# Performance work log

Measured on AMD Instinct MI355X. Metric: run time of the kernel, lower is better.

## Reference

```python
import jax, jax.numpy as jnp
import numpy as np

N_BINS = 25


def setup_inputs() -> dict:
    key = jax.random.key(0)
    k1, k2 = jax.random.split(key)
    logits = jax.random.normal(k1, (500000, 100), dtype=jnp.float32)
    labels = jax.random.randint(k2, (500000,), 0, 100, dtype=jnp.int64)
    return {"logits": logits, "labels": labels}


def reference(logits, labels):
    # softmax confidences + predictions
    probs = jax.nn.softmax(logits, axis=1)
    confidences = jnp.max(probs, axis=1)              # [N]
    predictions = jnp.argmax(probs, axis=1)           # [N]
    accuracies = (predictions == labels).astype(jnp.float32)

    # Equal-width bins over (0,1]: bin i covers (i/n_bins, (i+1)/n_bins].
    # conf > lower AND conf <= upper  <=>  bin = ceil(conf*n_bins)-1 (conf>0 always for softmax).
    bins = jnp.clip(jnp.ceil(confidences * N_BINS).astype(jnp.int32) - 1, 0, N_BINS - 1)

    counts = jax.ops.segment_sum(jnp.ones_like(confidences), bins, num_segments=N_BINS)
    sum_conf = jax.ops.segment_sum(confidences, bins, num_segments=N_BINS)
    sum_acc = jax.ops.segment_sum(accuracies, bins, num_segments=N_BINS)

    n = jnp.float32(confidences.shape[0])
    prop_in_bin = counts / n
    safe_counts = jnp.maximum(counts, 1.0)
    avg_conf = sum_conf / safe_counts
    avg_acc = sum_acc / safe_counts

    ece = jnp.sum(jnp.where(counts > 0, jnp.abs(avg_conf - avg_acc) * prop_in_bin, 0.0))
    return ece
```

## Files before the change

kernel.cpp:

```cpp
#include <hip/hip_runtime.h>
#include <cfloat>

#define NBINS 25
#define RPB   128
#define THREADS 256
#define GRID1 1024

__launch_bounds__(THREADS, 3)
__global__ void ece_pass1(const float* __restrict__ logits,
                          const int* __restrict__ labels,
                          float* __restrict__ part, int n) {
    __shared__ float tile[RPB * 100];
    __shared__ float s_cnt[NBINS], s_conf[NBINS], s_acc[NBINS];
    const int t = threadIdx.x;
    if (t < NBINS) { s_cnt[t] = 0.f; s_conf[t] = 0.f; s_acc[t] = 0.f; }

    const int j = t & 3;
    const int g = t >> 2;

    for (int c = blockIdx.x; c * RPB < n; c += GRID1) {
        const int base = c * RPB;
        const int rows = min(RPB, n - base);
        const int nf4  = rows * 25;

        const float4* src = reinterpret_cast<const float4*>(logits) + (size_t)base * 25;
        float4* dst = reinterpret_cast<float4*>(tile);
#pragma unroll
        for (int k = 0; k < 13; ++k) {
            const int idx = t + k * THREADS;
            if (idx < nf4) dst[idx] = src[idx];
        }
        __syncthreads();

#pragma unroll
        for (int rr = 0; rr < RPB; rr += 64) {
            const int r = rr + g;
            const float* rowp = tile + r * 100;
            float4 v[6];
#pragma unroll
            for (int k = 0; k < 6; ++k)
                v[k] = *reinterpret_cast<const float4*>(rowp + (j + 4 * k) * 4);
            const float x24 = rowp[96 + j];

            float m = v[0].x; int mi = 4 * j;
            if (v[0].y > m) { m = v[0].y; mi = 4 * j + 1; }
            if (v[0].z > m) { m = v[0].z; mi = 4 * j + 2; }
            if (v[0].w > m) { m = v[0].w; mi = 4 * j + 3; }
#pragma unroll
            for (int k = 1; k < 6; ++k) {
                const int idx = 4 * (j + 4 * k);
                if (v[k].x > m) { m = v[k].x; mi = idx; }
                if (v[k].y > m) { m = v[k].y; mi = idx + 1; }
                if (v[k].z > m) { m = v[k].z; mi = idx + 2; }
                if (v[k].w > m) { m = v[k].w; mi = idx + 3; }
            }
            if (x24 > m) { m = x24; mi = 96 + j; }
#pragma unroll
            for (int off = 1; off <= 2; off <<= 1) {
                const float om = __shfl_xor(m, off);
                const int   oi = __shfl_xor(mi, off);
                if (om > m || (om == m && oi < mi)) { m = om; mi = oi; }
            }
            float s = __expf(x24 - m);
#pragma unroll
            for (int k = 0; k < 6; ++k) {
                s += __expf(v[k].x - m) + __expf(v[k].y - m) +
                     __expf(v[k].z - m) + __expf(v[k].w - m);
            }
#pragma unroll
            for (int off = 1; off <= 2; off <<= 1) s += __shfl_xor(s, off);

            if (j == 0 && r < rows) {
                const float conf = 1.0f / s;
                int bin = (int)ceilf(conf * (float)NBINS) - 1;
                bin = min(max(bin, 0), NBINS - 1);
                const float acc = (mi == labels[base + r]) ? 1.f : 0.f;
                atomicAdd(&s_cnt[bin], 1.f);
                atomicAdd(&s_conf[bin], conf);
                atomicAdd(&s_acc[bin], acc);
            }
        }
        __syncthreads();
    }

    if (t < NBINS) {
        part[t * GRID1 + blockIdx.x]               = s_cnt[t];
        part[(NBINS + t) * GRID1 + blockIdx.x]     = s_conf[t];
        part[(2 * NBINS + t) * GRID1 + blockIdx.x] = s_acc[t];
    }
}

__global__ void ece_final(const float* __restrict__ part, float* __restrict__ out, float n) {
    __shared__ float sacc[3 * NBINS];
    const int t = threadIdx.x;
    const int wave = t >> 6, lane = t & 63;
    for (int slot = wave; slot < 3 * NBINS; slot += 16) {
        const float* p = part + slot * GRID1;
        float s = 0.f;
        for (int k = lane; k < GRID1; k += 64) s += p[k];
#pragma unroll
        for (int off = 32; off; off >>= 1) s += __shfl_xor(s, off);
        if (lane == 0) sacc[slot] = s;
    }
    __syncthreads();
    if (t < 64) {
        float term = 0.f;
        if (t < NBINS) {
            const float cnt = sacc[t];
            const float sc  = sacc[NBINS + t];
            const float sa  = sacc[2 * NBINS + t];
            if (cnt > 0.f) {
                const float inv = 1.f / cnt;
                term = fabsf(sc * inv - sa * inv) * (cnt / n);
            }
        }
#pragma unroll
        for (int off = 32; off; off >>= 1) term += __shfl_xor(term, off);
        if (t == 0) out[0] = term;
    }
}

extern "C" void kernel_launch(void* const* d_in, const int* in_sizes, int n_in,
                              void* d_out, int out_size, void* d_ws, size_t ws_size,
                              hipStream_t stream) {
    const float* logits = (const float*)d_in[0];
    const int*   labels = (const int*)d_in[1];
    float* part = (float*)d_ws;
    float* out  = (float*)d_out;
    const int n = in_sizes[1];

    ece_pass1<<<GRID1, THREADS, 0, stream>>>(logits, labels, part, n);
    ece_final<<<1, 1024, 0, stream>>>(part, out, (float)n);
}
```

Measured before the change: 334.7 us.

## Load logits directly into registers per wave instead of staging through LDS

Drops the shared-memory tile and the block-wide barrier around it. Each wave now owns a fixed range of 128 rows and loads two rows per 4-lane group straight from global memory into registers, so more loads are in flight. The launch bound asks for 4 blocks per CU instead of 3. The cost is strided per-lane float4 accesses that rely on cache-line reuse rather than fully coalesced staging, plus higher register pressure from holding two rows.

```diff
diff --git a/kernel.cpp b/kernel.cpp
--- a/kernel.cpp
+++ b/kernel.cpp
@@ -2,87 +2,93 @@
 #include <cfloat>
 
 #define NBINS 25
-#define RPB   128
 #define THREADS 256
 #define GRID1 1024
+#define ITERS 4
 
-__launch_bounds__(THREADS, 3)
+__device__ __forceinline__ void process_batch(const float4 v[7], int j, int lab, bool active,
+                                              float* s_cnt, float* s_conf, float* s_acc) {
+    const float x24 = (j == 0) ? v[6].x : (j == 1) ? v[6].y : (j == 2) ? v[6].z : v[6].w;
+
+    float m = v[0].x; int mi = 4 * j;
+    if (v[0].y > m) { m = v[0].y; mi = 4 * j + 1; }
+    if (v[0].z > m) { m = v[0].z; mi = 4 * j + 2; }
+    if (v[0].w > m) { m = v[0].w; mi = 4 * j + 3; }
+#pragma unroll
+    for (int k = 1; k < 6; ++k) {
+        const int idx = 4 * (j + 4 * k);
+        if (v[k].x > m) { m = v[k].x; mi = idx; }
+        if (v[k].y > m) { m = v[k].y; mi = idx + 1; }
+        if (v[k].z > m) { m = v[k].z; mi = idx + 2; }
+        if (v[k].w > m) { m = v[k].w; mi = idx + 3; }
+    }
+    if (x24 > m) { m = x24; mi = 96 + j; }
+#pragma unroll
+    for (int off = 1; off <= 2; off <<= 1) {
+        const float om = __shfl_xor(m, off);
+        const int   oi = __shfl_xor(mi, off);
+        if (om > m || (om == m && oi < mi)) { m = om; mi = oi; }
+    }
+    float s = __expf(x24 - m);
+#pragma unroll
+    for (int k = 0; k < 6; ++k) {
+        s += __expf(v[k].x - m) + __expf(v[k].y - m) +
+             __expf(v[k].z - m) + __expf(v[k].w - m);
+    }
+#pragma unroll
+    for (int off = 1; off <= 2; off <<= 1) s += __shfl_xor(s, off);
+
+    if (j == 0 && active) {
+        const float conf = 1.0f / s;
+        int bin = (int)ceilf(conf * (float)NBINS) - 1;
+        bin = min(max(bin, 0), NBINS - 1);
+        const float acc = (mi == lab) ? 1.f : 0.f;
+        atomicAdd(&s_cnt[bin], 1.f);
+        atomicAdd(&s_conf[bin], conf);
+        atomicAdd(&s_acc[bin], acc);
+    }
+}
+
+__launch_bounds__(THREADS, 4)
 __global__ void ece_pass1(const float* __restrict__ logits,
                           const int* __restrict__ labels,
                           float* __restrict__ part, int n) {
-    __shared__ float tile[RPB * 100];
     __shared__ float s_cnt[NBINS], s_conf[NBINS], s_acc[NBINS];
     const int t = threadIdx.x;
     if (t < NBINS) { s_cnt[t] = 0.f; s_conf[t] = 0.f; s_acc[t] = 0.f; }
+    __syncthreads();
 
-    const int j = t & 3;
-    const int g = t >> 2;
+    const int lane = t & 63;
+    const int j = lane & 3;
+    const int g = lane >> 2;
+    const int wid = (int)((blockIdx.x * THREADS + t) >> 6);
 
-    for (int c = blockIdx.x; c * RPB < n; c += GRID1) {
-        const int base = c * RPB;
-        const int rows = min(RPB, n - base);
-        const int nf4  = rows * 25;
+#pragma unroll 1
+    for (int it = 0; it < ITERS; ++it) {
+        const int rbase = wid * (ITERS * 32) + it * 32;
+        if (rbase >= n) break;
+        const int rowA = rbase + g;
+        const int rowB = rbase + 16 + g;
+        const int rA = min(rowA, n - 1);
+        const int rB = min(rowB, n - 1);
+        const float4* pA = reinterpret_cast<const float4*>(logits) + (size_t)rA * 25;
+        const float4* pB = reinterpret_cast<const float4*>(logits) + (size_t)rB * 25;
 
-        const float4* src = reinterpret_cast<const float4*>(logits) + (size_t)base * 25;
-        float4* dst = reinterpret_cast<float4*>(tile);
+        float4 va[7], vb[7];
 #pragma unroll
-        for (int k = 0; k < 13; ++k) {
-            const int idx = t + k * THREADS;
-            if (idx < nf4) dst[idx] = src[idx];
-        }
-        __syncthreads();
+        for (int k = 0; k < 6; ++k) va[k] = pA[j + 4 * k];
+        va[6] = pA[24];
+#pragma unroll
+        for (int k = 0; k < 6; ++k) vb[k] = pB[j + 4 * k];
+        vb[6] = pB[24];
+        const int labA = labels[rA];
+        const int labB = labels[rB];
 
-#pragma unroll
-        for (int rr = 0; rr < RPB; rr += 64) {
-            const int r = rr + g;
-            const float* rowp = tile + r * 100;
-            float4 v[6];
-#pragma unroll
-            for (int k = 0; k < 6; ++k)
-                v[k] = *reinterpret_cast<const float4*>(rowp + (j + 4 * k) * 4);
-            const float x24 = rowp[96 + j];
-
-            float m = v[0].x; int mi = 4 * j;
-            if (v[0].y > m) { m = v[0].y; mi = 4 * j + 1; }
-            if (v[0].z > m) { m = v[0].z; mi = 4 * j + 2; }
-            if (v[0].w > m) { m = v[0].w; mi = 4 * j + 3; }
-#pragma unroll
-            for (int k = 1; k < 6; ++k) {
-                const int idx = 4 * (j + 4 * k);
-                if (v[k].x > m) { m = v[k].x; mi = idx; }
-                if (v[k].y > m) { m = v[k].y; mi = idx + 1; }
-                if (v[k].z > m) { m = v[k].z; mi = idx + 2; }
-                if (v[k].w > m) { m = v[k].w; mi = idx + 3; }
-            }
-            if (x24 > m) { m = x24; mi = 96 + j; }
-#pragma unroll
-            for (int off = 1; off <= 2; off <<= 1) {
-                const float om = __shfl_xor(m, off);
-                const int   oi = __shfl_xor(mi, off);
-                if (om > m || (om == m && oi < mi)) { m = om; mi = oi; }
-            }
-            float s = __expf(x24 - m);
-#pragma unroll
-            for (int k = 0; k < 6; ++k) {
-                s += __expf(v[k].x - m) + __expf(v[k].y - m) +
-                     __expf(v[k].z - m) + __expf(v[k].w - m);
-            }
-#pragma unroll
-            for (int off = 1; off <= 2; off <<= 1) s += __shfl_xor(s, off);
-
-            if (j == 0 && r < rows) {
-                const float conf = 1.0f / s;
-                int bin = (int)ceilf(conf * (float)NBINS) - 1;
-                bin = min(max(bin, 0), NBINS - 1);
-                const float acc = (mi == labels[base + r]) ? 1.f : 0.f;
-                atomicAdd(&s_cnt[bin], 1.f);
-                atomicAdd(&s_conf[bin], conf);
-                atomicAdd(&s_acc[bin], acc);
-            }
-        }
-        __syncthreads();
+        process_batch(va, j, labA, rowA < n, s_cnt, s_conf, s_acc);
+        process_batch(vb, j, labB, rowB < n, s_cnt, s_conf, s_acc);
     }
 
+    __syncthreads();
     if (t < NBINS) {
         part[t * GRID1 + blockIdx.x]               = s_cnt[t];
         part[(NBINS + t) * GRID1 + blockIdx.x]     = s_conf[t];
```

Measured after the change: 382.4 us. 14.3% more time.

## Double-buffer logits tiles via direct global-to-LDS async loads

Applied to the files above, without the earlier changes.

Replaces the register-staged synchronous tile copy with __builtin_amdgcn_global_load_lds into two LDS buffers. The next 64-row chunk is prefetched while the current one is processed, synchronised with vmcnt waits and raw barriers. Labels are also staged into LDS, and grid and chunk sizes are retuned. The aim is to hide global-memory latency behind compute. The risks are fragile manual waitcnt accounting and smaller chunks, which mean more barriers per row.

```diff
diff --git a/kernel.cpp b/kernel.cpp
--- a/kernel.cpp
+++ b/kernel.cpp
@@ -1,59 +1,96 @@
 #include <hip/hip_runtime.h>
 #include <cfloat>
+#include <stdint.h>
 
 #define NBINS 25
-#define RPB   128
 #define THREADS 256
-#define GRID1 1024
+#define GRID1 768
+#define ROWS 64
+#define CH_F4 (ROWS * 25)
+
+#define GLOAD16(gp, lp)                                                     \
+    __builtin_amdgcn_global_load_lds(                                       \
+        (const __attribute__((address_space(1))) void*)(gp),                \
+        (__attribute__((address_space(3))) void*)(lp), 16, 0, 0)
+#define GLOAD4(gp, lp)                                                      \
+    __builtin_amdgcn_global_load_lds(                                       \
+        (const __attribute__((address_space(1))) void*)(gp),                \
+        (__attribute__((address_space(3))) void*)(lp), 4, 0, 0)
+#define VMCNT(N) asm volatile("s_waitcnt vmcnt(" #N ")" ::: "memory")
+
+#define ARGMAX_STEP(vk, k)                                                  \
+    { const int idx = 4 * (j + 4 * (k));                                    \
+      if ((vk).x > m) { m = (vk).x; mi = idx; }                             \
+      if ((vk).y > m) { m = (vk).y; mi = idx + 1; }                         \
+      if ((vk).z > m) { m = (vk).z; mi = idx + 2; }                         \
+      if ((vk).w > m) { m = (vk).w; mi = idx + 3; } }
 
 __launch_bounds__(THREADS, 3)
 __global__ void ece_pass1(const float* __restrict__ logits,
                           const int* __restrict__ labels,
                           float* __restrict__ part, int n) {
-    __shared__ float tile[RPB * 100];
+    __shared__ __align__(16) float tile[2][ROWS * 100];
+    __shared__ int labt[2][ROWS];
     __shared__ float s_cnt[NBINS], s_conf[NBINS], s_acc[NBINS];
     const int t = threadIdx.x;
     if (t < NBINS) { s_cnt[t] = 0.f; s_conf[t] = 0.f; s_acc[t] = 0.f; }
+    __syncthreads();
 
-    const int j = t & 3;
-    const int g = t >> 2;
+    const int w = t >> 6, l = t & 63;
+    const int j = l & 3, g = l >> 2;
+    const long totf4 = (long)n * 25;
+    const int NCHUNK = (n + ROWS - 1) / ROWS;
+    const float4* src = reinterpret_cast<const float4*>(logits);
 
-    for (int c = blockIdx.x; c * RPB < n; c += GRID1) {
-        const int base = c * RPB;
-        const int rows = min(RPB, n - base);
-        const int nf4  = rows * 25;
+    auto stage = [&](int buf, int c) {
+        const long cb = (long)c * CH_F4;
+        float* dst = tile[buf];
+        const int wb = w * 400;
+#pragma unroll
+        for (int k = 0; k < 6; ++k) {
+            long gi = cb + wb + k * 64 + l;
+            gi = gi < totf4 ? gi : (totf4 - 1);
+            GLOAD16(src + gi, dst + (size_t)(wb + k * 64 + l) * 4);
+        }
+        if (l < 16) {
+            long gi = cb + wb + 384 + l;
+            gi = gi < totf4 ? gi : (totf4 - 1);
+            GLOAD16(src + gi, dst + (size_t)(wb + 384 + l) * 4);
+        }
+        {
+            long gi = (long)c * ROWS + l;
+            gi = gi < n ? gi : (n - 1);
+            GLOAD4(labels + gi, labt[buf] + l);
+        }
+    };
 
-        const float4* src = reinterpret_cast<const float4*>(logits) + (size_t)base * 25;
-        float4* dst = reinterpret_cast<float4*>(tile);
-#pragma unroll
-        for (int k = 0; k < 13; ++k) {
-            const int idx = t + k * THREADS;
-            if (idx < nf4) dst[idx] = src[idx];
-        }
-        __syncthreads();
+    int c = blockIdx.x;
+    int cur = 0;
+    stage(0, c);
+    while (true) {
+        const int cn = c + GRID1;
+        const bool hn = cn < NCHUNK;
+        if (hn) { stage(cur ^ 1, cn); VMCNT(8); }
+        else    { VMCNT(0); }
+        __builtin_amdgcn_s_barrier();
 
-#pragma unroll
-        for (int rr = 0; rr < RPB; rr += 64) {
-            const int r = rr + g;
-            const float* rowp = tile + r * 100;
-            float4 v[6];
-#pragma unroll
-            for (int k = 0; k < 6; ++k)
-                v[k] = *reinterpret_cast<const float4*>(rowp + (j + 4 * k) * 4);
-            const float x24 = rowp[96 + j];
+        {
+            const int r  = w * 16 + g;
+            const int rg = c * ROWS + r;
+            const float* row = tile[cur] + r * 100;
+            const float4* r4 = reinterpret_cast<const float4*>(row);
+            const float4 v0 = r4[j];      const float4 v1 = r4[j + 4];
+            const float4 v2 = r4[j + 8];  const float4 v3 = r4[j + 12];
+            const float4 v4 = r4[j + 16]; const float4 v5 = r4[j + 20];
+            const float x24 = row[96 + j];
+            const int lab = labt[cur][r];
 
-            float m = v[0].x; int mi = 4 * j;
-            if (v[0].y > m) { m = v[0].y; mi = 4 * j + 1; }
-            if (v[0].z > m) { m = v[0].z; mi = 4 * j + 2; }
-            if (v[0].w > m) { m = v[0].w; mi = 4 * j + 3; }
-#pragma unroll
-            for (int k = 1; k < 6; ++k) {
-                const int idx = 4 * (j + 4 * k);
-                if (v[k].x > m) { m = v[k].x; mi = idx; }
-                if (v[k].y > m) { m = v[k].y; mi = idx + 1; }
-                if (v[k].z > m) { m = v[k].z; mi = idx + 2; }
-                if (v[k].w > m) { m = v[k].w; mi = idx + 3; }
-            }
+            float m = v0.x; int mi = 4 * j;
+            if (v0.y > m) { m = v0.y; mi = 4 * j + 1; }
+            if (v0.z > m) { m = v0.z; mi = 4 * j + 2; }
+            if (v0.w > m) { m = v0.w; mi = 4 * j + 3; }
+            ARGMAX_STEP(v1, 1) ARGMAX_STEP(v2, 2) ARGMAX_STEP(v3, 3)
+            ARGMAX_STEP(v4, 4) ARGMAX_STEP(v5, 5)
             if (x24 > m) { m = x24; mi = 96 + j; }
 #pragma unroll
             for (int off = 1; off <= 2; off <<= 1) {
@@ -62,27 +99,30 @@
                 if (om > m || (om == m && oi < mi)) { m = om; mi = oi; }
             }
             float s = __expf(x24 - m);
-#pragma unroll
-            for (int k = 0; k < 6; ++k) {
-                s += __expf(v[k].x - m) + __expf(v[k].y - m) +
-                     __expf(v[k].z - m) + __expf(v[k].w - m);
-            }
+            s += __expf(v0.x - m) + __expf(v0.y - m) + __expf(v0.z - m) + __expf(v0.w - m);
+            s += __expf(v1.x - m) + __expf(v1.y - m) + __expf(v1.z - m) + __expf(v1.w - m);
+            s += __expf(v2.x - m) + __expf(v2.y - m) + __expf(v2.z - m) + __expf(v2.w - m);
+            s += __expf(v3.x - m) + __expf(v3.y - m) + __expf(v3.z - m) + __expf(v3.w - m);
+            s += __expf(v4.x - m) + __expf(v4.y - m) + __expf(v4.z - m) + __expf(v4.w - m);
+            s += __expf(v5.x - m) + __expf(v5.y - m) + __expf(v5.z - m) + __expf(v5.w - m);
 #pragma unroll
             for (int off = 1; off <= 2; off <<= 1) s += __shfl_xor(s, off);
 
-            if (j == 0 && r < rows) {
+            if (j == 0 && rg < n) {
                 const float conf = 1.0f / s;
                 int bin = (int)ceilf(conf * (float)NBINS) - 1;
                 bin = min(max(bin, 0), NBINS - 1);
-                const float acc = (mi == labels[base + r]) ? 1.f : 0.f;
                 atomicAdd(&s_cnt[bin], 1.f);
                 atomicAdd(&s_conf[bin], conf);
-                atomicAdd(&s_acc[bin], acc);
+                atomicAdd(&s_acc[bin], (mi == lab) ? 1.f : 0.f);
             }
         }
-        __syncthreads();
+        __builtin_amdgcn_s_barrier();
+        if (!hn) break;
+        cur ^= 1; c = cn;
     }
 
+    __syncthreads();
     if (t < NBINS) {
         part[t * GRID1 + blockIdx.x]               = s_cnt[t];
         part[(NBINS + t) * GRID1 + blockIdx.x]     = s_conf[t];
```

New measurement: 298.1 us. 1.12x faster.
